# Kernel tuning notes

Measured on AMD Instinct MI355X. Metric: run time of the kernel, lower is better.

Reference implementation:

```python
import jax, jax.numpy as jnp
import numpy as np

ALPHA = 1.5
N_ITER = 50
B, N, C = 8, 1024, 1024
H = 8
D = C // H


def entmax_bisect(x, alpha=ALPHA, n_iter=N_ITER):
    # entmax-bisect (Peters et al. 2019), matching the entmax package's bisection.
    xm = (alpha - 1.0) * x
    d = xm.shape[-1]
    inv = 1.0 / (alpha - 1.0)  # = 2.0 for alpha=1.5
    max_val = jnp.max(xm, axis=-1, keepdims=True)
    tau_lo = max_val - 1.0                                   # gp(1, alpha) = 1
    tau_hi = max_val - (1.0 / d) ** (alpha - 1.0)            # gp(1/d, alpha)
    f_lo = jnp.sum(jnp.maximum(xm - tau_lo, 0.0) ** inv, axis=-1, keepdims=True) - 1.0
    dm0 = tau_hi - tau_lo

    def body(_, carry):
        tau_lo, dm, tau_m = carry
        dm = dm * 0.5
        tau_m = tau_lo + dm
        f_m = jnp.sum(jnp.maximum(xm - tau_m, 0.0) ** inv, axis=-1, keepdims=True) - 1.0
        tau_lo = jnp.where(f_m * f_lo >= 0, tau_m, tau_lo)
        return (tau_lo, dm, tau_m)

    _, _, tau_m = jax.lax.fori_loop(0, n_iter, body, (tau_lo, dm0, tau_lo))
    p = jnp.maximum(xm - tau_m, 0.0) ** inv
    return p / jnp.sum(p, axis=-1, keepdims=True)


def setup_inputs() -> dict:
    key = jax.random.key(0)
    ks = jax.random.split(key, 9)
    s = 0.02
    return {
        "x": jax.random.normal(ks[0], (B, N, C), dtype=jnp.float32),
        "Wq": jax.random.normal(ks[1], (C, C), dtype=jnp.float32) * s,
        "bq": jnp.zeros((C,), dtype=jnp.float32),
        "Wk": jax.random.normal(ks[2], (C, C), dtype=jnp.float32) * s,
        "bk": jnp.zeros((C,), dtype=jnp.float32),
        "Wv": jax.random.normal(ks[3], (C, C), dtype=jnp.float32) * s,
        "bv": jnp.zeros((C,), dtype=jnp.float32),
        "Wo": jax.random.normal(ks[4], (C, C), dtype=jnp.float32) * s,
        "bo": jnp.zeros((C,), dtype=jnp.float32),
    }


def reference(x, Wq, bq, Wk, bk, Wv, bv, Wo, bo):
    b, n, c = x.shape
    def proj(W, bias):
        return (x @ W + bias).reshape(b, n, H, D).transpose(0, 2, 1, 3)  # [B,H,N,D]
    q = proj(Wq, bq)
    k = proj(Wk, bk)
    v = proj(Wv, bv)
    scores = jnp.einsum("bhnd,bhmd->bhnm", q, k) / (D ** 0.5)  # [B,H,N,N]
    attn = entmax_bisect(scores)
    ctx = jnp.einsum("bhnm,bhmd->bhnd", attn, v)
    ctx = ctx.transpose(0, 2, 1, 3).reshape(b, n, c)
    out = ctx @ Wo + bo
    return (out, attn)
```

## Files before the change

kernel.cpp:

```cpp
#include <hip/hip_runtime.h>

#define DEV __device__ __forceinline__

typedef _Float16 f16;
typedef _Float16 f16x8 __attribute__((ext_vector_type(8)));
typedef float f32x4 __attribute__((ext_vector_type(4)));


DEV void gload_lds16(const f16* g, f16* l) {
  __builtin_amdgcn_global_load_lds(
      (const __attribute__((address_space(1))) void*)g,
      (__attribute__((address_space(3))) void*)l, 16, 0, 0);
}


__global__ __launch_bounds__(256) void cast_f32_f16(const float* __restrict__ in,
                                                    f16* __restrict__ out, int n) {
  int i = (blockIdx.x * 256 + threadIdx.x) * 4;
  if (i < n) {
    float4 f = *(const float4*)(in + i);
    f16 o0 = (f16)f.x, o1 = (f16)f.y, o2 = (f16)f.z, o3 = (f16)f.w;
    f16* d = out + i;
    d[0] = o0; d[1] = o1; d[2] = o2; d[3] = o3;
  }
}

__global__ __launch_bounds__(256) void transpose_cast(
    const float* s0, const float* s1, const float* s2, const float* s3,
    f16* d0, f16* d1, f16* d2, f16* d3) {
  const float* S[4] = {s0, s1, s2, s3};
  f16* D[4] = {d0, d1, d2, d3};
  const float* W = S[blockIdx.z];
  f16* WT = D[blockIdx.z];
  __shared__ float tile[32][33];
  int tx = threadIdx.x, ty = threadIdx.y;
  int r0 = blockIdx.y * 32, c0 = blockIdx.x * 32;
#pragma unroll
  for (int i = 0; i < 32; i += 8) tile[ty + i][tx] = W[(r0 + ty + i) * 1024 + c0 + tx];
  __syncthreads();
#pragma unroll
  for (int i = 0; i < 32; i += 8) WT[(c0 + ty + i) * 1024 + r0 + tx] = (f16)tile[tx][ty + i];
}


DEV void gemm_bt_f16(const f16* __restrict__ A, const f16* __restrict__ B,
                     int lda, int ldb, int K, f16* As, f16* Bs, f32x4 (&acc)[4][4]) {
  const int t = threadIdx.x;
  const int l = t & 63, w = t >> 6;
  const int wm = w >> 1, wn = w & 1;
  const f16* ag = A + (t >> 2) * lda + (t & 3) * 8;
  const f16* bg = B + (t >> 2) * ldb + (t & 3) * 8;
  f16* asd = As + w * 512;
  f16* bsd = Bs + w * 512;
  const int arow = wm * 64 + (l & 15);
  const int brow = wn * 64 + (l & 15);
  const int ko = (l >> 4) * 8;
  for (int k0 = 0; k0 < K; k0 += 32) {
    __syncthreads();
    gload_lds16(ag + k0, asd);
    gload_lds16(ag + 64 * lda + k0, asd + 2048);
    gload_lds16(bg + k0, bsd);
    gload_lds16(bg + 64 * ldb + k0, bsd + 2048);
    __syncthreads();
    f16x8 af[4], bf[4];
#pragma unroll
    for (int i = 0; i < 4; i++) af[i] = *(const f16x8*)(As + (arow + i * 16) * 32 + ko);
#pragma unroll
    for (int j = 0; j < 4; j++) bf[j] = *(const f16x8*)(Bs + (brow + j * 16) * 32 + ko);
#pragma unroll
    for (int i = 0; i < 4; i++)
#pragma unroll
      for (int j = 0; j < 4; j++)
        acc[i][j] = __builtin_amdgcn_mfma_f32_16x16x32_f16(af[i], bf[j], acc[i][j], 0, 0, 0);
  }
}


__global__ __launch_bounds__(256) void qkv_gemm(
    const f16* __restrict__ xb, const f16* __restrict__ WTq, const f16* __restrict__ WTk,
    const f16* __restrict__ WTv, const float* __restrict__ bq, const float* __restrict__ bk,
    const float* __restrict__ bv, f16* __restrict__ q, f16* __restrict__ kk,
    f16* __restrict__ vT) {
  __shared__ f16 As[128 * 32];
  __shared__ f16 Bs[128 * 32];
  __shared__ f16 tr[128 * 132];
  const int z = blockIdx.z;
  const f16* WT = (z == 0) ? WTq : ((z == 1) ? WTk : WTv);
  const float* bias = (z == 0) ? bq : ((z == 1) ? bk : bv);
  const int rowBase = blockIdx.y * 128, colBase = blockIdx.x * 128;
  f32x4 zero4 = {0.f, 0.f, 0.f, 0.f};
  f32x4 acc[4][4];
#pragma unroll
  for (int i = 0; i < 4; i++)
#pragma unroll
    for (int j = 0; j < 4; j++) acc[i][j] = zero4;
  gemm_bt_f16(xb + rowBase * 1024, WT + colBase * 1024, 1024, 1024, 1024, As, Bs, acc);
  const int t = threadIdx.x, l = t & 63, w = t >> 6, wm = w >> 1, wn = w & 1;
  if (z < 2) {
    f16* dst = (z == 0) ? q : kk;
#pragma unroll
    for (int i = 0; i < 4; i++)
#pragma unroll
      for (int j = 0; j < 4; j++)
#pragma unroll
        for (int r = 0; r < 4; r++) {
          int rt = wm * 64 + i * 16 + ((l >> 4) << 2) + r;
          int ct = wn * 64 + j * 16 + (l & 15);
          int rr = rowBase + rt, c = colBase + ct;
          float val = acc[i][j][r] + bias[c];
          int b = rr >> 10, n = rr & 1023, h = c >> 7, d = c & 127;
          dst[((b * 8 + h) * 1024 + n) * 128 + d] = (f16)val;
        }
  } else {
#pragma unroll
    for (int i = 0; i < 4; i++)
#pragma unroll
      for (int j = 0; j < 4; j++)
#pragma unroll
        for (int r = 0; r < 4; r++) {
          int rt = wm * 64 + i * 16 + ((l >> 4) << 2) + r;
          int ct = wn * 64 + j * 16 + (l & 15);
          tr[ct * 132 + rt] = (f16)(acc[i][j][r] + bias[colBase + ct]);
        }
    __syncthreads();
    int b = blockIdx.y >> 3, h = blockIdx.x;
    int nb = (blockIdx.y & 7) * 128;
    int head = b * 8 + h;
#pragma unroll
    for (int p = 0; p < 8; p++) {
      int lin = p * 2048 + t * 8;
      int c = lin >> 7, r = lin & 127;
      const f16* src = &tr[c * 132 + r];
      uint2 a0 = *(const uint2*)(src);
      uint2 a1 = *(const uint2*)(src + 4);
      f16* dst = vT + head * 131072 + c * 1024 + nb + r;
      *(uint2*)(dst) = a0;
      *(uint2*)(dst + 4) = a1;
    }
  }
}


#define PSLD 1032

__global__ __launch_bounds__(512, 4) void fused_attn(
    const f16* __restrict__ q, const f16* __restrict__ kk,
    const f16* __restrict__ vT, float* __restrict__ attn, f16* __restrict__ ctx) {
  __shared__ f16 Ps[32 * PSLD];
  const int t = threadIdx.x, l = t & 63, w = t >> 6;
  const int blk = blockIdx.x;
  const int xcd = blk & 7;
  const int slot = blk >> 3;
  const int head = xcd * 8 + (slot >> 5);
  const int n0 = (slot & 31) * 32;
  const int l15 = l & 15, l16 = l >> 4;
  const int bb = head >> 3, hh = head & 7;
  const float SC = 0.04419417382415922f;

  const f16* qh = q + head * 131072;
  const f16* kh = kk + head * 131072;
  const f16* vh = vT + head * 131072;

  f16x8 qf[2][4];
#pragma unroll
  for (int mt = 0; mt < 2; mt++)
#pragma unroll
    for (int kb = 0; kb < 4; kb++)
      qf[mt][kb] = *(const f16x8*)(qh + (n0 + mt * 16 + l15) * 128 + kb * 32 + l16 * 8);

#pragma unroll 4
  for (int i = 0; i < 8; i++) {
    const int nt = w * 8 + i;
    f16x8 bf[4];
#pragma unroll
    for (int kb = 0; kb < 4; kb++)
      bf[kb] = *(const f16x8*)(kh + (nt * 16 + l15) * 128 + kb * 32 + l16 * 8);
    f32x4 acc[2] = {{0.f, 0.f, 0.f, 0.f}, {0.f, 0.f, 0.f, 0.f}};
#pragma unroll
    for (int mt = 0; mt < 2; mt++)
#pragma unroll
      for (int kb = 0; kb < 4; kb++)
        acc[mt] = __builtin_amdgcn_mfma_f32_16x16x32_f16(qf[mt][kb], bf[kb], acc[mt], 0, 0, 0);
#pragma unroll
    for (int mt = 0; mt < 2; mt++)
#pragma unroll
      for (int r = 0; r < 4; r++)
        Ps[(mt * 16 + l16 * 4 + r) * PSLD + nt * 16 + l15] = (f16)(acc[mt][r] * SC);
  }
  __syncthreads();

  for (int p = 0; p < 2; p++) {
    f16* r0p = Ps + (size_t)(w * 4 + p * 2) * PSLD;
    f16* r1p = r0p + PSLD;
    f16x8 a0 = *(const f16x8*)(r0p + l * 8);
    f16x8 a1 = *(const f16x8*)(r0p + 512 + l * 8);
    f16x8 c0 = *(const f16x8*)(r1p + l * 8);
    f16x8 c1 = *(const f16x8*)(r1p + 512 + l * 8);
    float x0[16], x1[16];
#pragma unroll
    for (int e = 0; e < 8; e++) {
      x0[e] = (float)a0[e]; x0[8 + e] = (float)a1[e];
      x1[e] = (float)c0[e]; x1[8 + e] = (float)c1[e];
    }
    float m0 = x0[0], m1 = x1[0];
#pragma unroll
    for (int e = 1; e < 16; e++) { m0 = fmaxf(m0, x0[e]); m1 = fmaxf(m1, x1[e]); }
#pragma unroll
    for (int o = 32; o; o >>= 1) {
      m0 = fmaxf(m0, __shfl_xor(m0, o, 64));
      m1 = fmaxf(m1, __shfl_xor(m1, o, 64));
    }
    float lo0 = m0 - 1.0f, lo1 = m1 - 1.0f;
    float dm = 0.96875f;
    float tm0 = lo0, tm1 = lo1;
    for (int it = 0; it < 13; ++it) {
      dm *= 0.5f;
      tm0 = lo0 + dm; tm1 = lo1 + dm;
      float a0s = 0.f, a1s = 0.f;
#pragma unroll
      for (int e = 0; e < 16; e++) {
        float a = fmaxf(x0[e] - tm0, 0.f); a0s = fmaf(a, a, a0s);
        float b = fmaxf(x1[e] - tm1, 0.f); a1s = fmaf(b, b, a1s);
      }
#pragma unroll
      for (int o = 32; o; o >>= 1) { a0s += __shfl_xor(a0s, o, 64); a1s += __shfl_xor(a1s, o, 64); }
      if (a0s >= 1.0f) lo0 = tm0;
      if (a1s >= 1.0f) lo1 = tm1;
    }
    float q0 = 0.f, q1 = 0.f;
#pragma unroll
    for (int e = 0; e < 16; e++) {
      float a = fmaxf(x0[e] - tm0, 0.f); x0[e] = a * a; q0 += x0[e];
      float b = fmaxf(x1[e] - tm1, 0.f); x1[e] = b * b; q1 += x1[e];
    }
#pragma unroll
    for (int o = 32; o; o >>= 1) { q0 += __shfl_xor(q0, o, 64); q1 += __shfl_xor(q1, o, 64); }
    float i0 = 1.0f / q0, i1 = 1.0f / q1;
    float* a0p = attn + ((size_t)head * 1024 + n0 + w * 4 + p * 2) * 1024;
    float* a1p = a0p + 1024;
    float4 v0 = {x0[0] * i0, x0[1] * i0, x0[2] * i0, x0[3] * i0};
    float4 v1 = {x0[4] * i0, x0[5] * i0, x0[6] * i0, x0[7] * i0};
    float4 v2 = {x0[8] * i0, x0[9] * i0, x0[10] * i0, x0[11] * i0};
    float4 v3 = {x0[12] * i0, x0[13] * i0, x0[14] * i0, x0[15] * i0};
    float4 u0 = {x1[0] * i1, x1[1] * i1, x1[2] * i1, x1[3] * i1};
    float4 u1 = {x1[4] * i1, x1[5] * i1, x1[6] * i1, x1[7] * i1};
    float4 u2 = {x1[8] * i1, x1[9] * i1, x1[10] * i1, x1[11] * i1};
    float4 u3 = {x1[12] * i1, x1[13] * i1, x1[14] * i1, x1[15] * i1};
    *(float4*)(a0p + l * 8) = v0;
    *(float4*)(a0p + l * 8 + 4) = v1;
    *(float4*)(a0p + 512 + l * 8) = v2;
    *(float4*)(a0p + 512 + l * 8 + 4) = v3;
    *(float4*)(a1p + l * 8) = u0;
    *(float4*)(a1p + l * 8 + 4) = u1;
    *(float4*)(a1p + 512 + l * 8) = u2;
    *(float4*)(a1p + 512 + l * 8 + 4) = u3;
    f16x8 o0 = {(f16)v0.x, (f16)v0.y, (f16)v0.z, (f16)v0.w,
                (f16)v1.x, (f16)v1.y, (f16)v1.z, (f16)v1.w};
    f16x8 o1 = {(f16)v2.x, (f16)v2.y, (f16)v2.z, (f16)v2.w,
                (f16)v3.x, (f16)v3.y, (f16)v3.z, (f16)v3.w};
    f16x8 o2 = {(f16)u0.x, (f16)u0.y, (f16)u0.z, (f16)u0.w,
                (f16)u1.x, (f16)u1.y, (f16)u1.z, (f16)u1.w};
    f16x8 o3 = {(f16)u2.x, (f16)u2.y, (f16)u2.z, (f16)u2.w,
                (f16)u3.x, (f16)u3.y, (f16)u3.z, (f16)u3.w};
    *(f16x8*)(r0p + l * 8) = o0;
    *(f16x8*)(r0p + 512 + l * 8) = o1;
    *(f16x8*)(r1p + l * 8) = o2;
    *(f16x8*)(r1p + 512 + l * 8) = o3;
  }
  __syncthreads();

  f32x4 cacc[2] = {{0.f, 0.f, 0.f, 0.f}, {0.f, 0.f, 0.f, 0.f}};
#pragma unroll 8
  for (int kb = 0; kb < 32; kb++) {
    f16x8 bfv = *(const f16x8*)(vh + (w * 16 + l15) * 1024 + kb * 32 + l16 * 8);
    f16x8 af0 = *(const f16x8*)(Ps + l15 * PSLD + kb * 32 + l16 * 8);
    f16x8 af1 = *(const f16x8*)(Ps + (16 + l15) * PSLD + kb * 32 + l16 * 8);
    cacc[0] = __builtin_amdgcn_mfma_f32_16x16x32_f16(af0, bfv, cacc[0], 0, 0, 0);
    cacc[1] = __builtin_amdgcn_mfma_f32_16x16x32_f16(af1, bfv, cacc[1], 0, 0, 0);
  }
#pragma unroll
  for (int mt = 0; mt < 2; mt++)
#pragma unroll
    for (int r = 0; r < 4; r++) {
      int m = mt * 16 + l16 * 4 + r;
      int d = w * 16 + l15;
      ctx[(size_t)(bb * 1024 + n0 + m) * 1024 + hh * 128 + d] = (f16)cacc[mt][r];
    }
}


__global__ __launch_bounds__(256) void out_gemm(const f16* __restrict__ ctx,
                                                const f16* __restrict__ WTo,
                                                const float* __restrict__ bo,
                                                float* __restrict__ out) {
  __shared__ f16 As[128 * 32];
  __shared__ f16 Bs[128 * 32];
  const int rowBase = blockIdx.y * 128, colBase = blockIdx.x * 128;
  f32x4 zero4 = {0.f, 0.f, 0.f, 0.f};
  f32x4 acc[4][4];
#pragma unroll
  for (int i = 0; i < 4; i++)
#pragma unroll
    for (int j = 0; j < 4; j++) acc[i][j] = zero4;
  gemm_bt_f16(ctx + rowBase * 1024, WTo + colBase * 1024, 1024, 1024, 1024, As, Bs, acc);
  const int l = threadIdx.x & 63, w = threadIdx.x >> 6, wm = w >> 1, wn = w & 1;
#pragma unroll
  for (int i = 0; i < 4; i++)
#pragma unroll
    for (int j = 0; j < 4; j++)
#pragma unroll
      for (int r = 0; r < 4; r++) {
        int rt = wm * 64 + i * 16 + ((l >> 4) << 2) + r;
        int ct = wn * 64 + j * 16 + (l & 15);
        out[(size_t)(rowBase + rt) * 1024 + colBase + ct] = acc[i][j][r] + bo[colBase + ct];
      }
}


extern "C" void kernel_launch(void* const* d_in, const int* in_sizes, int n_in,
                              void* d_out, int out_size, void* d_ws, size_t ws_size,
                              hipStream_t stream) {
  const float* x  = (const float*)d_in[0];
  const float* Wq = (const float*)d_in[1];
  const float* bq = (const float*)d_in[2];
  const float* Wk = (const float*)d_in[3];
  const float* bk = (const float*)d_in[4];
  const float* Wv = (const float*)d_in[5];
  const float* bv = (const float*)d_in[6];
  const float* Wo = (const float*)d_in[7];
  const float* bo = (const float*)d_in[8];
  float* out = (float*)d_out;
  float* attn = out + 8388608;

  char* ws = (char*)d_ws;
  f16* xb  = (f16*)(ws);
  f16* ctx = (f16*)(ws);
  f16* WTq = (f16*)(ws + (16u << 20));
  f16* WTk = (f16*)(ws + (18u << 20));
  f16* WTv = (f16*)(ws + (20u << 20));
  f16* WTo = (f16*)(ws + (22u << 20));
  f16* q   = (f16*)(ws + (24u << 20));
  f16* kk  = (f16*)(ws + (40u << 20));
  f16* vT  = (f16*)(ws + (56u << 20));

  cast_f32_f16<<<dim3(8192), dim3(256), 0, stream>>>(x, xb, 8388608);
  transpose_cast<<<dim3(32, 32, 4), dim3(32, 8), 0, stream>>>(
      Wq, Wk, Wv, Wo, WTq, WTk, WTv, WTo);
  qkv_gemm<<<dim3(8, 64, 3), dim3(256), 0, stream>>>(
      xb, WTq, WTk, WTv, bq, bk, bv, q, kk, vT);
  fused_attn<<<dim3(2048), dim3(512), 0, stream>>>(q, kk, vT, attn, ctx);
  out_gemm<<<dim3(8, 64), dim3(256), 0, stream>>>(ctx, WTo, bo, out);
}
```

Before: 605.5 us.

## Use packed f16 bisection, vectorize cast/transpose and qkv epilogue stores

The entmax bisection now runs on packed half2 values using packed max and fdot2 accumulation, with one fewer iteration. The cast and weight-transpose kernels now use wider tiles and vector stores. The q/k epilogue stages results through LDS so it can write coalesced 16-byte rows, and bias loads are hoisted. These changes target ALU cost in the bisection loop and uncoalesced narrow stores, at the cost of reduced threshold precision (f16 tau) and fewer bisection steps, which risks accuracy.

Result: faster. 582.8 us (-3.7%).

```diff
diff --git a/kernel.cpp b/kernel.cpp
--- a/kernel.cpp
+++ b/kernel.cpp
@@ -4,7 +4,17 @@
 
 typedef _Float16 f16;
 typedef _Float16 f16x8 __attribute__((ext_vector_type(8)));
+typedef _Float16 f16x4 __attribute__((ext_vector_type(4)));
+typedef _Float16 h2 __attribute__((ext_vector_type(2)));
 typedef float f32x4 __attribute__((ext_vector_type(4)));
+
+#if __has_builtin(__builtin_amdgcn_fdot2)
+#define FDOT2(a, b, c) __builtin_amdgcn_fdot2((a), (b), (c), false)
+#else
+DEV float FDOT2(h2 a, h2 b, float c) {
+  return c + (float)a[0] * (float)b[0] + (float)a[1] * (float)b[1];
+}
+#endif
 
 
 DEV void gload_lds16(const f16* g, f16* l) {
@@ -16,12 +26,13 @@
 
 __global__ __launch_bounds__(256) void cast_f32_f16(const float* __restrict__ in,
                                                     f16* __restrict__ out, int n) {
-  int i = (blockIdx.x * 256 + threadIdx.x) * 4;
+  int i = (blockIdx.x * 256 + threadIdx.x) * 8;
   if (i < n) {
-    float4 f = *(const float4*)(in + i);
-    f16 o0 = (f16)f.x, o1 = (f16)f.y, o2 = (f16)f.z, o3 = (f16)f.w;
-    f16* d = out + i;
-    d[0] = o0; d[1] = o1; d[2] = o2; d[3] = o3;
+    float4 f0 = *(const float4*)(in + i);
+    float4 f1 = *(const float4*)(in + i + 4);
+    f16x8 o = {(f16)f0.x, (f16)f0.y, (f16)f0.z, (f16)f0.w,
+               (f16)f1.x, (f16)f1.y, (f16)f1.z, (f16)f1.w};
+    *(f16x8*)(out + i) = o;
   }
 }
 
@@ -32,14 +43,23 @@
   f16* D[4] = {d0, d1, d2, d3};
   const float* W = S[blockIdx.z];
   f16* WT = D[blockIdx.z];
-  __shared__ float tile[32][33];
-  int tx = threadIdx.x, ty = threadIdx.y;
-  int r0 = blockIdx.y * 32, c0 = blockIdx.x * 32;
-#pragma unroll
-  for (int i = 0; i < 32; i += 8) tile[ty + i][tx] = W[(r0 + ty + i) * 1024 + c0 + tx];
+  __shared__ float tile[64 * 66];
+  const int t = threadIdx.x;
+  const int r0 = blockIdx.y * 64, c0 = blockIdx.x * 64;
+  const int lr = t >> 6, lc = t & 63;
+#pragma unroll
+  for (int i = 0; i < 16; i++)
+    tile[(i * 4 + lr) * 66 + lc] = W[(r0 + i * 4 + lr) * 1024 + c0 + lc];
   __syncthreads();
-#pragma unroll
-  for (int i = 0; i < 32; i += 8) WT[(c0 + ty + i) * 1024 + r0 + tx] = (f16)tile[tx][ty + i];
+  const int wc = t >> 4;
+  const int wr4 = (t & 15) * 4;
+#pragma unroll
+  for (int j = 0; j < 4; j++) {
+    int cc = j * 16 + wc;
+    f16x4 pk = {(f16)tile[(wr4 + 0) * 66 + cc], (f16)tile[(wr4 + 1) * 66 + cc],
+                (f16)tile[(wr4 + 2) * 66 + cc], (f16)tile[(wr4 + 3) * 66 + cc]};
+    *(f16x4*)(WT + (size_t)(c0 + cc) * 1024 + r0 + wr4) = pk;
+  }
 }
 
 
@@ -83,7 +103,7 @@
     f16* __restrict__ vT) {
   __shared__ f16 As[128 * 32];
   __shared__ f16 Bs[128 * 32];
-  __shared__ f16 tr[128 * 132];
+  __shared__ f16 tr[128 * 136];
   const int z = blockIdx.z;
   const f16* WT = (z == 0) ? WTq : ((z == 1) ? WTk : WTv);
   const float* bias = (z == 0) ? bq : ((z == 1) ? bk : bv);
@@ -96,6 +116,12 @@
     for (int j = 0; j < 4; j++) acc[i][j] = zero4;
   gemm_bt_f16(xb + rowBase * 1024, WT + colBase * 1024, 1024, 1024, 1024, As, Bs, acc);
   const int t = threadIdx.x, l = t & 63, w = t >> 6, wm = w >> 1, wn = w & 1;
+  const int b = blockIdx.y >> 3, h = blockIdx.x;
+  const int nb = (blockIdx.y & 7) * 128;
+  const int head = b * 8 + h;
+  float b4[4];
+#pragma unroll
+  for (int j = 0; j < 4; j++) b4[j] = bias[colBase + wn * 64 + j * 16 + (l & 15)];
   if (z < 2) {
     f16* dst = (z == 0) ? q : kk;
 #pragma unroll
@@ -106,11 +132,17 @@
         for (int r = 0; r < 4; r++) {
           int rt = wm * 64 + i * 16 + ((l >> 4) << 2) + r;
           int ct = wn * 64 + j * 16 + (l & 15);
-          int rr = rowBase + rt, c = colBase + ct;
-          float val = acc[i][j][r] + bias[c];
-          int b = rr >> 10, n = rr & 1023, h = c >> 7, d = c & 127;
-          dst[((b * 8 + h) * 1024 + n) * 128 + d] = (f16)val;
+          tr[rt * 136 + ct] = (f16)(acc[i][j][r] + b4[j]);
         }
+    __syncthreads();
+    f16* dstb = dst + ((size_t)head * 1024 + nb) * 128;
+#pragma unroll
+    for (int p = 0; p < 8; p++) {
+      int lin = p * 2048 + t * 8;
+      int rt = lin >> 7, ct = lin & 127;
+      f16x8 v = *(const f16x8*)(&tr[rt * 136 + ct]);
+      *(f16x8*)(dstb + lin) = v;
+    }
   } else {
 #pragma unroll
     for (int i = 0; i < 4; i++)
@@ -120,22 +152,15 @@
         for (int r = 0; r < 4; r++) {
           int rt = wm * 64 + i * 16 + ((l >> 4) << 2) + r;
           int ct = wn * 64 + j * 16 + (l & 15);
-          tr[ct * 132 + rt] = (f16)(acc[i][j][r] + bias[colBase + ct]);
+          tr[ct * 136 + rt] = (f16)(acc[i][j][r] + b4[j]);
         }
     __syncthreads();
-    int b = blockIdx.y >> 3, h = blockIdx.x;
-    int nb = (blockIdx.y & 7) * 128;
-    int head = b * 8 + h;
 #pragma unroll
     for (int p = 0; p < 8; p++) {
       int lin = p * 2048 + t * 8;
       int c = lin >> 7, r = lin & 127;
-      const f16* src = &tr[c * 132 + r];
-      uint2 a0 = *(const uint2*)(src);
-      uint2 a1 = *(const uint2*)(src + 4);
-      f16* dst = vT + head * 131072 + c * 1024 + nb + r;
-      *(uint2*)(dst) = a0;
-      *(uint2*)(dst + 4) = a1;
+      f16x8 v = *(const f16x8*)(&tr[c * 136 + r]);
+      *(f16x8*)(vT + head * 131072 + c * 1024 + nb + r) = v;
     }
   }
 }
@@ -189,22 +214,30 @@
   }
   __syncthreads();
 
+  const h2 z2 = {(f16)0.f, (f16)0.f};
   for (int p = 0; p < 2; p++) {
     f16* r0p = Ps + (size_t)(w * 4 + p * 2) * PSLD;
     f16* r1p = r0p + PSLD;
-    f16x8 a0 = *(const f16x8*)(r0p + l * 8);
-    f16x8 a1 = *(const f16x8*)(r0p + 512 + l * 8);
-    f16x8 c0 = *(const f16x8*)(r1p + l * 8);
-    f16x8 c1 = *(const f16x8*)(r1p + 512 + l * 8);
-    float x0[16], x1[16];
-#pragma unroll
-    for (int e = 0; e < 8; e++) {
-      x0[e] = (float)a0[e]; x0[8 + e] = (float)a1[e];
-      x1[e] = (float)c0[e]; x1[8 + e] = (float)c1[e];
-    }
-    float m0 = x0[0], m1 = x1[0];
-#pragma unroll
-    for (int e = 1; e < 16; e++) { m0 = fmaxf(m0, x0[e]); m1 = fmaxf(m1, x1[e]); }
+    f16x8 A0 = *(const f16x8*)(r0p + l * 8);
+    f16x8 A1 = *(const f16x8*)(r0p + 512 + l * 8);
+    f16x8 B0 = *(const f16x8*)(r1p + l * 8);
+    f16x8 B1 = *(const f16x8*)(r1p + 512 + l * 8);
+    h2 a[8], b[8];
+#pragma unroll
+    for (int e = 0; e < 4; e++) {
+      a[e] = h2{A0[2 * e], A0[2 * e + 1]};
+      a[e + 4] = h2{A1[2 * e], A1[2 * e + 1]};
+      b[e] = h2{B0[2 * e], B0[2 * e + 1]};
+      b[e + 4] = h2{B1[2 * e], B1[2 * e + 1]};
+    }
+    h2 ma = a[0], mb = b[0];
+#pragma unroll
+    for (int e = 1; e < 8; e++) {
+      ma = __builtin_elementwise_max(ma, a[e]);
+      mb = __builtin_elementwise_max(mb, b[e]);
+    }
+    float m0 = fmaxf((float)ma[0], (float)ma[1]);
+    float m1 = fmaxf((float)mb[0], (float)mb[1]);
 #pragma unroll
     for (int o = 32; o; o >>= 1) {
       m0 = fmaxf(m0, __shfl_xor(m0, o, 64));
@@ -213,39 +246,52 @@
     float lo0 = m0 - 1.0f, lo1 = m1 - 1.0f;
     float dm = 0.96875f;
     float tm0 = lo0, tm1 = lo1;
-    for (int it = 0; it < 13; ++it) {
+    for (int it = 0; it < 12; ++it) {
       dm *= 0.5f;
       tm0 = lo0 + dm; tm1 = lo1 + dm;
-      float a0s = 0.f, a1s = 0.f;
-#pragma unroll
-      for (int e = 0; e < 16; e++) {
-        float a = fmaxf(x0[e] - tm0, 0.f); a0s = fmaf(a, a, a0s);
-        float b = fmaxf(x1[e] - tm1, 0.f); a1s = fmaf(b, b, a1s);
+      f16 th0 = (f16)tm0, th1 = (f16)tm1;
+      h2 t0 = {th0, th0}, t1 = {th1, th1};
+      float s0 = 0.f, s1 = 0.f;
+#pragma unroll
+      for (int e = 0; e < 8; e++) {
+        h2 d0 = __builtin_elementwise_max(a[e] - t0, z2);
+        h2 d1 = __builtin_elementwise_max(b[e] - t1, z2);
+        s0 = FDOT2(d0, d0, s0);
+        s1 = FDOT2(d1, d1, s1);
       }
 #pragma unroll
-      for (int o = 32; o; o >>= 1) { a0s += __shfl_xor(a0s, o, 64); a1s += __shfl_xor(a1s, o, 64); }
-      if (a0s >= 1.0f) lo0 = tm0;
-      if (a1s >= 1.0f) lo1 = tm1;
-    }
+      for (int o = 32; o; o >>= 1) { s0 += __shfl_xor(s0, o, 64); s1 += __shfl_xor(s1, o, 64); }
+      if (s0 >= 1.0f) lo0 = tm0;
+      if (s1 >= 1.0f) lo1 = tm1;
+    }
+    f16 th0 = (f16)tm0, th1 = (f16)tm1;
+    h2 t0 = {th0, th0}, t1 = {th1, th1};
+    float pa[16], pb[16];
     float q0 = 0.f, q1 = 0.f;
 #pragma unroll
-    for (int e = 0; e < 16; e++) {
-      float a = fmaxf(x0[e] - tm0, 0.f); x0[e] = a * a; q0 += x0[e];
-      float b = fmaxf(x1[e] - tm1, 0.f); x1[e] = b * b; q1 += x1[e];
+    for (int e = 0; e < 8; e++) {
+      h2 d0 = __builtin_elementwise_max(a[e] - t0, z2);
+      h2 d1 = __builtin_elementwise_max(b[e] - t1, z2);
+      float f0 = (float)d0[0], f1 = (float)d0[1];
+      float g0 = (float)d1[0], g1 = (float)d1[1];
+      pa[2 * e] = f0 * f0; pa[2 * e + 1] = f1 * f1;
+      pb[2 * e] = g0 * g0; pb[2 * e + 1] = g1 * g1;
+      q0 += pa[2 * e] + pa[2 * e + 1];
+      q1 += pb[2 * e] + pb[2 * e + 1];
     }
 #pragma unroll
     for (int o = 32; o; o >>= 1) { q0 += __shfl_xor(q0, o, 64); q1 += __shfl_xor(q1, o, 64); }
     float i0 = 1.0f / q0, i1 = 1.0f / q1;
     float* a0p = attn + ((size_t)head * 1024 + n0 + w * 4 + p * 2) * 1024;
     float* a1p = a0p + 1024;
-    float4 v0 = {x0[0] * i0, x0[1] * i0, x0[2] * i0, x0[3] * i0};
-    float4 v1 = {x0[4] * i0, x0[5] * i0, x0[6] * i0, x0[7] * i0};
-    float4 v2 = {x0[8] * i0, x0[9] * i0, x0[10] * i0, x0[11] * i0};
-    float4 v3 = {x0[12] * i0, x0[13] * i0, x0[14] * i0, x0[15] * i0};
-    float4 u0 = {x1[0] * i1, x1[1] * i1, x1[2] * i1, x1[3] * i1};
-    float4 u1 = {x1[4] * i1, x1[5] * i1, x1[6] * i1, x1[7] * i1};
-    float4 u2 = {x1[8] * i1, x1[9] * i1, x1[10] * i1, x1[11] * i1};
-    float4 u3 = {x1[12] * i1, x1[13] * i1, x1[14] * i1, x1[15] * i1};
+    float4 v0 = {pa[0] * i0, pa[1] * i0, pa[2] * i0, pa[3] * i0};
+    float4 v1 = {pa[4] * i0, pa[5] * i0, pa[6] * i0, pa[7] * i0};
+    float4 v2 = {pa[8] * i0, pa[9] * i0, pa[10] * i0, pa[11] * i0};
+    float4 v3 = {pa[12] * i0, pa[13] * i0, pa[14] * i0, pa[15] * i0};
+    float4 u0 = {pb[0] * i1, pb[1] * i1, pb[2] * i1, pb[3] * i1};
+    float4 u1 = {pb[4] * i1, pb[5] * i1, pb[6] * i1, pb[7] * i1};
+    float4 u2 = {pb[8] * i1, pb[9] * i1, pb[10] * i1, pb[11] * i1};
+    float4 u3 = {pb[12] * i1, pb[13] * i1, pb[14] * i1, pb[15] * i1};
     *(float4*)(a0p + l * 8) = v0;
     *(float4*)(a0p + l * 8 + 4) = v1;
     *(float4*)(a0p + 512 + l * 8) = v2;
@@ -343,8 +389,8 @@
   f16* kk  = (f16*)(ws + (40u << 20));
   f16* vT  = (f16*)(ws + (56u << 20));
 
-  cast_f32_f16<<<dim3(8192), dim3(256), 0, stream>>>(x, xb, 8388608);
-  transpose_cast<<<dim3(32, 32, 4), dim3(32, 8), 0, stream>>>(
+  cast_f32_f16<<<dim3(4096), dim3(256), 0, stream>>>(x, xb, 8388608);
+  transpose_cast<<<dim3(16, 16, 4), dim3(256), 0, stream>>>(
       Wq, Wk, Wv, Wo, WTq, WTk, WTv, WTo);
   qkv_gemm<<<dim3(8, 64, 3), dim3(256), 0, stream>>>(
       xb, WTq, WTk, WTv, bq, bk, bv, q, kk, vT);
```
